# Kernel tuning notes

Hardware: AMD Instinct MI355X
Metric: run time of the kernel (lower is better)

## Reference

```python
import jax, jax.numpy as jnp
import numpy as np

B, N, C, K = 4, 4096, 64, 16
EPS = 1e-5


def _bn(x, g, b, m, v):
    # eval-mode BatchNorm2d on [B, C, N, K]
    scale = (g / jnp.sqrt(v + EPS))[None, :, None, None]
    return (x - m[None, :, None, None]) * scale + b[None, :, None, None]


def setup_inputs() -> dict:
    key = jax.random.key(0)
    ks = jax.random.split(key, 32)
    s = 0.05
    inp = {
        "p": jax.random.normal(ks[0], (B, N, 3), jnp.float32),
        "x": jax.random.normal(ks[1], (B, C, N), jnp.float32),
        "mask": jnp.ones((B, N), dtype=bool),
        # q/k/v 1x1 Conv1d weights [out, in] + bias
        "Wq": jax.random.normal(ks[2], (C, C)) * s, "bq": jax.random.normal(ks[3], (C,)) * s,
        "Wk": jax.random.normal(ks[4], (C, C)) * s, "bk": jax.random.normal(ks[5], (C,)) * s,
        "Wv": jax.random.normal(ks[6], (C, C)) * s, "bv": jax.random.normal(ks[7], (C,)) * s,
        # pos-enc: Conv2d(3->C, no bias), BN, ReLU, Conv2d(C->C)
        "pe_w1": jax.random.normal(ks[8], (C, 3)) * s,
        "pe_bn_g": jax.random.normal(ks[9], (C,)) * s + 1.0,
        "pe_bn_b": jax.random.normal(ks[10], (C,)) * s,
        "pe_bn_m": jax.random.normal(ks[11], (C,)) * s,
        "pe_bn_v": jax.random.uniform(ks[12], (C,), minval=0.5, maxval=1.5),
        "pe_w2": jax.random.normal(ks[13], (C, C)) * s, "pe_b2": jax.random.normal(ks[14], (C,)) * s,
        # attn: BN, ReLU, Conv2d(C->C, no bias), BN, ReLU, Conv2d(C->C)
        "at_bn0_g": jax.random.normal(ks[15], (C,)) * s + 1.0,
        "at_bn0_b": jax.random.normal(ks[16], (C,)) * s,
        "at_bn0_m": jax.random.normal(ks[17], (C,)) * s,
        "at_bn0_v": jax.random.uniform(ks[18], (C,), minval=0.5, maxval=1.5),
        "at_w1": jax.random.normal(ks[19], (C, C)) * s,
        "at_bn1_g": jax.random.normal(ks[20], (C,)) * s + 1.0,
        "at_bn1_b": jax.random.normal(ks[21], (C,)) * s,
        "at_bn1_m": jax.random.normal(ks[22], (C,)) * s,
        "at_bn1_v": jax.random.uniform(ks[23], (C,), minval=0.5, maxval=1.5),
        "at_w2": jax.random.normal(ks[24], (C, C)) * s, "at_b2": jax.random.normal(ks[25], (C,)) * s,
    }
    return inp


def reference(p, x, mask, Wq, bq, Wk, bk, Wv, bv,
              pe_w1, pe_bn_g, pe_bn_b, pe_bn_m, pe_bn_v, pe_w2, pe_b2,
              at_bn0_g, at_bn0_b, at_bn0_m, at_bn0_v, at_w1,
              at_bn1_g, at_bn1_b, at_bn1_m, at_bn1_v, at_w2, at_b2):
    # q, k, v: 1x1 Conv1d -> [B, C, N]
    q = jnp.einsum('oc,bcn->bon', Wq, x) + bq[None, :, None]
    k = jnp.einsum('oc,bcn->bon', Wk, x) + bk[None, :, None]
    v = jnp.einsum('oc,bcn->bon', Wv, x) + bv[None, :, None]

    # ---- knn_point(K, p, p): Euclidean cdist, zero-point masking, topk smallest
    sq = jnp.sum(p * p, axis=-1)                                   # [B, N]
    d2 = sq[:, :, None] + sq[:, None, :] - 2.0 * jnp.einsum('bnc,bmc->bnm', p, p)
    dist = jnp.sqrt(jnp.maximum(d2, 0.0))                          # [B, N, N]
    valid = ~jnp.all(p == 0, axis=-1)                              # [B, N]
    dist = jnp.where(valid[:, None, :], dist, jnp.inf)
    _, idx = jax.lax.top_k(-dist, K)                               # [B, N, K]

    gather = jax.vmap(lambda a, i: a[i])                           # ([N,C],[N,K]) -> [N,K,C]
    n_k = gather(jnp.transpose(k, (0, 2, 1)), idx)                 # [B, N, K, C]
    n_v = gather(jnp.transpose(v, (0, 2, 1)), idx)                 # [B, N, K, C]
    n_p = gather(p, idx)                                           # [B, N, K, 3]

    rel = p[:, :, None, :] - n_p                                   # [B, N, K, 3]
    rel = jnp.transpose(rel, (0, 3, 1, 2))                         # [B, 3, N, K]

    # position encoding MLP
    h = jnp.einsum('oc,bcnk->bonk', pe_w1, rel)
    h = jax.nn.relu(_bn(h, pe_bn_g, pe_bn_b, pe_bn_m, pe_bn_v))
    n_r = jnp.einsum('oc,bcnk->bonk', pe_w2, h) + pe_b2[None, :, None, None]  # [B,C,N,K]

    # attention MLP on (q - n_k + n_r)
    a = q[:, :, :, None] - jnp.transpose(n_k, (0, 3, 1, 2)) + n_r
    a = jax.nn.relu(_bn(a, at_bn0_g, at_bn0_b, at_bn0_m, at_bn0_v))
    a = jnp.einsum('oc,bcnk->bonk', at_w1, a)
    a = jax.nn.relu(_bn(a, at_bn1_g, at_bn1_b, at_bn1_m, at_bn1_v))
    a = jnp.einsum('oc,bcnk->bonk', at_w2, a) + at_b2[None, :, None, None]

    # mask [B,N] broadcast to [B,C,N,K] (masks query rows, as in original)
    a = jnp.where(mask[:, None, :, None], a, -1e10)
    a = jax.nn.softmax(a, axis=-1)
    a = jnp.where(jnp.isnan(a), 0.0, a)

    y = jnp.sum(a * (jnp.transpose(n_v, (0, 3, 1, 2)) + n_r), axis=-1)  # [B, C, N]
    return (p, y)
```

## Files before the change

kernel.cpp:

```cpp
#include <hip/hip_runtime.h>
#include <stdint.h>

#define NB 4
#define NP 4096
#define NC 64
#define NK 16
#define BN_EPS 1e-5f

typedef __attribute__((ext_vector_type(8))) short short8;
typedef __attribute__((ext_vector_type(4))) float f32x4;
typedef unsigned long long u64;

__device__ __forceinline__ short f2bf(float f) {
    unsigned u = __float_as_uint(f);
    unsigned r = (u + 0x7FFFu + ((u >> 16) & 1u)) >> 16;
    return (short)(unsigned short)r;
}

__global__ __launch_bounds__(256) void px_kernel(const float* __restrict__ p,
                                                 float4* __restrict__ px,
                                                 float* __restrict__ pcopy) {
    int gid = blockIdx.x * 256 + threadIdx.x;
    float x = p[gid * 3 + 0], y = p[gid * 3 + 1], z = p[gid * 3 + 2];
    pcopy[gid * 3 + 0] = x; pcopy[gid * 3 + 1] = y; pcopy[gid * 3 + 2] = z;
    float sq = fmaf(z, z, fmaf(y, y, x * x));
    bool inv = (x == 0.0f) && (y == 0.0f) && (z == 0.0f);
    px[gid] = make_float4(x, y, z, inv ? __builtin_inff() : sq);
}

__global__ __launch_bounds__(256) void qkv_kernel(
        const float* __restrict__ x,
        const float* __restrict__ Wq, const float* __restrict__ bq,
        const float* __restrict__ Wk, const float* __restrict__ bk,
        const float* __restrict__ Wv, const float* __restrict__ bv,
        float* __restrict__ outbase) {
    __shared__ float wt[NC * NC];
    __shared__ float bsh[NC];
    const int which = blockIdx.y;
    const float* W    = which == 0 ? Wq : which == 1 ? Wk : Wv;
    const float* bias = which == 0 ? bq : which == 1 ? bk : bv;
    float* out = outbase + (size_t)which * NB * NP * NC;

    for (int e = threadIdx.x; e < NC * NC; e += 256)
        wt[(e & 63) * NC + (e >> 6)] = W[e];
    if (threadIdx.x < NC) bsh[threadIdx.x] = bias[threadIdx.x];
    __syncthreads();

    const int gid   = blockIdx.x * 256 + threadIdx.x;
    const int token = gid & (NB * NP - 1);
    const int qtr   = gid >> 14;
    const int b = token >> 12, n = token & (NP - 1);

    float acc[16];
#pragma unroll
    for (int o = 0; o < 16; ++o) acc[o] = bsh[qtr * 16 + o];

    const float* xp = x + (size_t)b * NC * NP + n;
#pragma unroll 4
    for (int c = 0; c < NC; ++c) {
        float xc = xp[(size_t)c * NP];
        const float4* wr = (const float4*)&wt[c * NC + qtr * 16];
#pragma unroll
        for (int o4 = 0; o4 < 4; ++o4) {
            float4 w4 = wr[o4];
            acc[o4 * 4 + 0] = fmaf(w4.x, xc, acc[o4 * 4 + 0]);
            acc[o4 * 4 + 1] = fmaf(w4.y, xc, acc[o4 * 4 + 1]);
            acc[o4 * 4 + 2] = fmaf(w4.z, xc, acc[o4 * 4 + 2]);
            acc[o4 * 4 + 3] = fmaf(w4.w, xc, acc[o4 * 4 + 3]);
        }
    }
    float4* op = (float4*)(out + (size_t)token * NC + qtr * 16);
#pragma unroll
    for (int o4 = 0; o4 < 4; ++o4)
        op[o4] = make_float4(acc[o4 * 4 + 0], acc[o4 * 4 + 1],
                             acc[o4 * 4 + 2], acc[o4 * 4 + 3]);
}

#define KQW 4
#define KCAP 64

__global__ __launch_bounds__(256) void knn_kernel(const float4* __restrict__ px,
                                                  int* __restrict__ idxout) {
    __shared__ float tb[4][KQW * 64];
    __shared__ u64 sbuf[16][KCAP];
    __shared__ int scnt[16];
    const int l = threadIdx.x & 63;
    const int w = threadIdx.x >> 6;
    const int gw = blockIdx.x * 4 + w;
    const int q0 = gw * KQW;
    const int b  = q0 >> 12;
    const float4* pb = px + (size_t)b * NP;

    float4 pn[KQW];
#pragma unroll
    for (int j = 0; j < KQW; ++j) pn[j] = px[q0 + j];
    if (l < KQW) scnt[w * KQW + l] = 0;
    __builtin_amdgcn_wave_barrier();

    float k1[KQW];
#pragma unroll
    for (int j = 0; j < KQW; ++j) k1[j] = __builtin_inff();
#pragma unroll 4
    for (int i = 0; i < NP / 64; ++i) {
        float4 pm = pb[i * 64 + l];
#pragma unroll
        for (int j = 0; j < KQW; ++j) {
            float dot = fmaf(pm.z, pn[j].z, fmaf(pm.y, pn[j].y, pm.x * pn[j].x));
            float d2 = fmaxf((pn[j].w + pm.w) - 2.0f * dot, 0.0f);
            k1[j] = fminf(k1[j], d2);
        }
    }
#pragma unroll
    for (int j = 0; j < KQW; ++j) tb[w][j * 64 + l] = k1[j];
    __builtin_amdgcn_wave_barrier();

    float T[KQW];
#pragma unroll
    for (int j = 0; j < KQW; ++j) {
        const float* tj = &tb[w][j * 64];
        int rank = 0;
#pragma unroll 4
        for (int t = 0; t < 64; t += 4) {
            f32x4 v = *(const f32x4*)&tj[t];
            rank += (v[0] < k1[j]) + (v[1] < k1[j]) + (v[2] < k1[j]) + (v[3] < k1[j]);
        }
        float cand = (rank <= 15) ? k1[j] : -__builtin_inff();
#pragma unroll
        for (int off = 32; off; off >>= 1)
            cand = fmaxf(cand, __shfl_xor(cand, off));
        T[j] = cand;
    }

#pragma unroll 2
    for (int i = 0; i < NP / 64; ++i) {
        int m = i * 64 + l;
        float4 pm = pb[m];
#pragma unroll
        for (int j = 0; j < KQW; ++j) {
            float dot = fmaf(pm.z, pn[j].z, fmaf(pm.y, pn[j].y, pm.x * pn[j].x));
            float d2 = fmaxf((pn[j].w + pm.w) - 2.0f * dot, 0.0f);
            if (d2 <= T[j]) {
                int pos = atomicAdd(&scnt[w * KQW + j], 1);
                if (pos < KCAP)
                    sbuf[w * KQW + j][pos] =
                        ((u64)__float_as_uint(d2) << 32) | (unsigned int)m;
            }
        }
    }
    __builtin_amdgcn_wave_barrier();

#pragma unroll 1
    for (int j = 0; j < KQW; ++j) {
        int cnt = scnt[w * KQW + j];
        if (cnt > KCAP) cnt = KCAP;
        if (l < cnt) {
            const u64* sb = sbuf[w * KQW + j];
            u64 kj = sb[l];
            int rank = 0;
            for (int t = 0; t < cnt; ++t) rank += (sb[t] < kj);
            if (rank < NK)
                idxout[(size_t)(q0 + j) * NK + rank] = (int)(kj & 0xffffffffu);
        }
    }
}

#define QPW 4
#define HBSTR 72
#define DBSTR 20

__device__ __forceinline__ short8 pack8(float4 a, float4 b) {
    short8 r;
    r[0] = f2bf(a.x); r[1] = f2bf(a.y); r[2] = f2bf(a.z); r[3] = f2bf(a.w);
    r[4] = f2bf(b.x); r[5] = f2bf(b.y); r[6] = f2bf(b.z); r[7] = f2bf(b.w);
    return r;
}

__device__ __forceinline__ void gemm_stage(const short8* wf ,
                                           const unsigned short* HBw,
                                           float* DBw, int tok, int quad) {
    short8 b0 = *(const short8*)((const char*)HBw + tok * (HBSTR * 2) + quad * 16);
    short8 b1 = *(const short8*)((const char*)HBw + tok * (HBSTR * 2) + 64 + quad * 16);
#pragma unroll
    for (int ob = 0; ob < 4; ++ob) {
        f32x4 acc = {0.0f, 0.0f, 0.0f, 0.0f};
        acc = __builtin_amdgcn_mfma_f32_16x16x32_bf16(wf[ob * 2 + 0], b0, acc, 0, 0, 0);
        acc = __builtin_amdgcn_mfma_f32_16x16x32_bf16(wf[ob * 2 + 1], b1, acc, 0, 0, 0);
#pragma unroll
        for (int r = 0; r < 4; ++r)
            DBw[(ob * 16 + quad * 4 + r) * DBSTR + tok] = acc[r];
    }
}

__global__ __launch_bounds__(64, 2) void fused_mfma_kernel(
        const float4* __restrict__ px, const int* __restrict__ idx,
        const float* __restrict__ qT, const float* __restrict__ kT,
        const float* __restrict__ vT,
        const float* __restrict__ pe_w1,
        const float* __restrict__ pe_g, const float* __restrict__ pe_b,
        const float* __restrict__ pe_m, const float* __restrict__ pe_v,
        const float* __restrict__ pe_w2, const float* __restrict__ pe_b2,
        const float* __restrict__ b0g, const float* __restrict__ b0b,
        const float* __restrict__ b0m, const float* __restrict__ b0v,
        const float* __restrict__ at_w1,
        const float* __restrict__ b1g, const float* __restrict__ b1b,
        const float* __restrict__ b1m, const float* __restrict__ b1v,
        const float* __restrict__ at_w2, const float* __restrict__ at_b2,
        float* __restrict__ yout) {
    __shared__ __align__(16) unsigned short HBw[16 * HBSTR];
    __shared__ __align__(16) float DBw[64 * DBSTR];

    const int l    = threadIdx.x;
    const int c    = l;
    const int tok  = l & 15;
    const int quad = l >> 4;

    short8 wf[3][8];
    {
        const float* Ws[3] = {pe_w2, at_w1, at_w2};
#pragma unroll
        for (int mat = 0; mat < 3; ++mat)
#pragma unroll
            for (int ob = 0; ob < 4; ++ob)
#pragma unroll
                for (int ch = 0; ch < 2; ++ch) {
                    const float* src = Ws[mat] + (ob * 16 + tok) * NC + ch * 32 + quad * 8;
                    float4 a = *(const float4*)src;
                    float4 bq4 = *(const float4*)(src + 4);
                    wf[mat][ob * 2 + ch] = pack8(a, bq4);
                }
    }

    const float pw0 = pe_w1[c * 3 + 0], pw1 = pe_w1[c * 3 + 1], pw2v = pe_w1[c * 3 + 2];
    const float pes = pe_g[c] / sqrtf(pe_v[c] + BN_EPS);
    const float peb = fmaf(-pe_m[c], pes, pe_b[c]);
    const float s0  = b0g[c] / sqrtf(b0v[c] + BN_EPS);
    const float bb0 = fmaf(-b0m[c], s0, b0b[c]);
    const float s1  = b1g[c] / sqrtf(b1v[c] + BN_EPS);
    const float bb1 = fmaf(-b1m[c], s1, b1b[c]);
    const float peb2 = pe_b2[c];
    const float ab2  = at_b2[c];

    const int gw = blockIdx.x;

    for (int jq = 0; jq < QPW; ++jq) {
        const int qi = gw * QPW + jq;
        const int b = qi >> 12, n = qi & (NP - 1);
        const float4 pn = px[qi];
        const float qv = qT[(size_t)qi * NC + c];

        const int4* ip = (const int4*)(idx + (size_t)qi * NK);
        int4 nid0 = ip[0], nid1 = ip[1], nid2 = ip[2], nid3 = ip[3];
        int mreg[NK] = {nid0.x, nid0.y, nid0.z, nid0.w,
                        nid1.x, nid1.y, nid1.z, nid1.w,
                        nid2.x, nid2.y, nid2.z, nid2.w,
                        nid3.x, nid3.y, nid3.z, nid3.w};

        float4 pmr[NK];
#pragma unroll
        for (int k = 0; k < NK; ++k) pmr[k] = px[b * NP + mreg[k]];

#pragma unroll
        for (int k = 0; k < NK; ++k) {
            float r0 = pn.x - pmr[k].x, r1 = pn.y - pmr[k].y, r2 = pn.z - pmr[k].z;
            float h = fmaf(pw2v, r2, fmaf(pw1, r1, pw0 * r0));
            h = fmaxf(fmaf(h, pes, peb), 0.0f);
            HBw[k * HBSTR + c] = (unsigned short)f2bf(h);
        }
        __builtin_amdgcn_wave_barrier();

        float kreg[NK];
#pragma unroll
        for (int k = 0; k < NK; ++k)
            kreg[k] = kT[((size_t)(b * NP + mreg[k])) * NC + c];

        gemm_stage(wf[0], HBw, DBw, tok, quad);
        __builtin_amdgcn_wave_barrier();

        float nr[NK];
#pragma unroll
        for (int j = 0; j < 4; ++j) {
            f32x4 v4 = *(const f32x4*)(DBw + c * DBSTR + j * 4);
            nr[j * 4 + 0] = v4[0] + peb2;
            nr[j * 4 + 1] = v4[1] + peb2;
            nr[j * 4 + 2] = v4[2] + peb2;
            nr[j * 4 + 3] = v4[3] + peb2;
        }
        __builtin_amdgcn_wave_barrier();

#pragma unroll
        for (int k = 0; k < NK; ++k) {
            float a0 = qv - kreg[k] + nr[k];
            a0 = fmaxf(fmaf(a0, s0, bb0), 0.0f);
            HBw[k * HBSTR + c] = (unsigned short)f2bf(a0);
        }
        __builtin_amdgcn_wave_barrier();

        float vreg[NK];
#pragma unroll
        for (int k = 0; k < NK; ++k)
            vreg[k] = vT[((size_t)(b * NP + mreg[k])) * NC + c];

        gemm_stage(wf[1], HBw, DBw, tok, quad);
        __builtin_amdgcn_wave_barrier();

#pragma unroll
        for (int j = 0; j < 4; ++j) {
            f32x4 v4 = *(const f32x4*)(DBw + c * DBSTR + j * 4);
#pragma unroll
            for (int r = 0; r < 4; ++r) {
                float a2 = fmaxf(fmaf(v4[r], s1, bb1), 0.0f);
                HBw[(j * 4 + r) * HBSTR + c] = (unsigned short)f2bf(a2);
            }
        }
        __builtin_amdgcn_wave_barrier();

        gemm_stage(wf[2], HBw, DBw, tok, quad);
        __builtin_amdgcn_wave_barrier();

        float a3[NK];
#pragma unroll
        for (int j = 0; j < 4; ++j) {
            f32x4 v4 = *(const f32x4*)(DBw + c * DBSTR + j * 4);
            a3[j * 4 + 0] = v4[0] + ab2;
            a3[j * 4 + 1] = v4[1] + ab2;
            a3[j * 4 + 2] = v4[2] + ab2;
            a3[j * 4 + 3] = v4[3] + ab2;
        }
        __builtin_amdgcn_wave_barrier();

        float mx = a3[0];
#pragma unroll
        for (int k = 1; k < NK; ++k) mx = fmaxf(mx, a3[k]);
        float ssum = 0.0f, yacc = 0.0f;
#pragma unroll
        for (int k = 0; k < NK; ++k) {
            float e = __expf(a3[k] - mx);
            ssum += e;
            yacc = fmaf(e, vreg[k] + nr[k], yacc);
        }
        yout[((size_t)(b * NC + c)) * NP + n] = yacc / ssum;
        __builtin_amdgcn_wave_barrier();
    }
}

extern "C" void kernel_launch(void* const* d_in, const int* in_sizes, int n_in,
                              void* d_out, int out_size, void* d_ws, size_t ws_size,
                              hipStream_t stream) {
    const float* p    = (const float*)d_in[0];
    const float* x    = (const float*)d_in[1];
    const float* Wq = (const float*)d_in[3];  const float* bq = (const float*)d_in[4];
    const float* Wk = (const float*)d_in[5];  const float* bk = (const float*)d_in[6];
    const float* Wv = (const float*)d_in[7];  const float* bv = (const float*)d_in[8];
    const float* pe_w1 = (const float*)d_in[9];
    const float* pe_g  = (const float*)d_in[10]; const float* pe_b = (const float*)d_in[11];
    const float* pe_m  = (const float*)d_in[12]; const float* pe_v = (const float*)d_in[13];
    const float* pe_w2 = (const float*)d_in[14]; const float* pe_b2 = (const float*)d_in[15];
    const float* b0g = (const float*)d_in[16]; const float* b0b = (const float*)d_in[17];
    const float* b0m = (const float*)d_in[18]; const float* b0v = (const float*)d_in[19];
    const float* at_w1 = (const float*)d_in[20];
    const float* b1g = (const float*)d_in[21]; const float* b1b = (const float*)d_in[22];
    const float* b1m = (const float*)d_in[23]; const float* b1v = (const float*)d_in[24];
    const float* at_w2 = (const float*)d_in[25]; const float* at_b2 = (const float*)d_in[26];

    const size_t BNC = (size_t)NB * NP * NC;
    float* ws  = (float*)d_ws;
    float* qT  = ws;
    float* kT  = qT + BNC;
    float* vT  = kT + BNC;
    float4* px = (float4*)(vT + BNC);
    int* idx   = (int*)(px + (size_t)NB * NP);

    float* outp = (float*)d_out;
    float* y = outp + (size_t)NB * NP * 3;

    px_kernel<<<dim3(64), dim3(256), 0, stream>>>(p, px, outp);
    qkv_kernel<<<dim3(256, 3), dim3(256), 0, stream>>>(x, Wq, bq, Wk, bk, Wv, bv, qT);
    knn_kernel<<<dim3(1024), dim3(256), 0, stream>>>(px, idx);
    fused_mfma_kernel<<<dim3(4096), dim3(64), 0, stream>>>(
        px, idx, qT, kT, vT, pe_w1, pe_g, pe_b, pe_m, pe_v, pe_w2, pe_b2,
        b0g, b0b, b0m, b0v, at_w1, b1g, b1b, b1m, b1v, at_w2, at_b2, y);
}
```

Baseline: 225.8 us.

## Share bf16 weight fragments in LDS across four waves per block

The fused kernel now runs 256-thread blocks of four waves. Three of the waves cooperatively pack the three 64x64 weight matrices into bf16 MFMA fragments in LDS, and every wave reads its A operands from there instead of holding 24 short8 fragments in registers. This frees registers to raise occupancy and amortises the weight loads across four waves. Smaller changes split the neighbour-point gather into two halves, recompute the final logits from LDS instead of keeping a 16-float array, and remap queries so a block covers a single batch. In exchange it adds LDS reads for the weights on every MFMA and a block-wide barrier after setup.

```diff
diff --git a/kernel.cpp b/kernel.cpp
--- a/kernel.cpp
+++ b/kernel.cpp
@@ -175,23 +175,26 @@
     return r;
 }
 
-__device__ __forceinline__ void gemm_stage(const short8* wf ,
-                                           const unsigned short* HBw,
-                                           float* DBw, int tok, int quad) {
+__device__ __forceinline__ void gemm_stage_lds(const short8 (*__restrict__ WFm)[64],
+                                               int l,
+                                               const unsigned short* HBw,
+                                               float* DBw, int tok, int quad) {
     short8 b0 = *(const short8*)((const char*)HBw + tok * (HBSTR * 2) + quad * 16);
     short8 b1 = *(const short8*)((const char*)HBw + tok * (HBSTR * 2) + 64 + quad * 16);
 #pragma unroll
     for (int ob = 0; ob < 4; ++ob) {
         f32x4 acc = {0.0f, 0.0f, 0.0f, 0.0f};
-        acc = __builtin_amdgcn_mfma_f32_16x16x32_bf16(wf[ob * 2 + 0], b0, acc, 0, 0, 0);
-        acc = __builtin_amdgcn_mfma_f32_16x16x32_bf16(wf[ob * 2 + 1], b1, acc, 0, 0, 0);
+        short8 a0 = WFm[ob * 2 + 0][l];
+        short8 a1 = WFm[ob * 2 + 1][l];
+        acc = __builtin_amdgcn_mfma_f32_16x16x32_bf16(a0, b0, acc, 0, 0, 0);
+        acc = __builtin_amdgcn_mfma_f32_16x16x32_bf16(a1, b1, acc, 0, 0, 0);
 #pragma unroll
         for (int r = 0; r < 4; ++r)
             DBw[(ob * 16 + quad * 4 + r) * DBSTR + tok] = acc[r];
     }
 }
 
-__global__ __launch_bounds__(64, 2) void fused_mfma_kernel(
+__global__ __launch_bounds__(256, 3) void fused_mfma_kernel(
         const float4* __restrict__ px, const int* __restrict__ idx,
         const float* __restrict__ qT, const float* __restrict__ kT,
         const float* __restrict__ vT,
@@ -206,28 +209,26 @@
         const float* __restrict__ b1m, const float* __restrict__ b1v,
         const float* __restrict__ at_w2, const float* __restrict__ at_b2,
         float* __restrict__ yout) {
-    __shared__ __align__(16) unsigned short HBw[16 * HBSTR];
-    __shared__ __align__(16) float DBw[64 * DBSTR];
-
-    const int l    = threadIdx.x;
+    __shared__ __align__(16) short8 WFl[3][8][64];
+    __shared__ __align__(16) char UB[4][64 * DBSTR * 4];
+
+    const int l    = threadIdx.x & 63;
+    const int w    = threadIdx.x >> 6;
     const int c    = l;
     const int tok  = l & 15;
     const int quad = l >> 4;
 
-    short8 wf[3][8];
-    {
-        const float* Ws[3] = {pe_w2, at_w1, at_w2};
-#pragma unroll
-        for (int mat = 0; mat < 3; ++mat)
-#pragma unroll
-            for (int ob = 0; ob < 4; ++ob)
-#pragma unroll
-                for (int ch = 0; ch < 2; ++ch) {
-                    const float* src = Ws[mat] + (ob * 16 + tok) * NC + ch * 32 + quad * 8;
-                    float4 a = *(const float4*)src;
-                    float4 bq4 = *(const float4*)(src + 4);
-                    wf[mat][ob * 2 + ch] = pack8(a, bq4);
-                }
+    if (w < 3) {
+        const float* Wm = w == 0 ? pe_w2 : w == 1 ? at_w1 : at_w2;
+#pragma unroll
+        for (int ob = 0; ob < 4; ++ob)
+#pragma unroll
+            for (int ch = 0; ch < 2; ++ch) {
+                const float* src = Wm + (ob * 16 + tok) * NC + ch * 32 + quad * 8;
+                float4 a = *(const float4*)src;
+                float4 bq4 = *(const float4*)(src + 4);
+                WFl[w][ob * 2 + ch][l] = pack8(a, bq4);
+            }
     }
 
     const float pw0 = pe_w1[c * 3 + 0], pw1 = pe_w1[c * 3 + 1], pw2v = pe_w1[c * 3 + 2];
@@ -240,10 +241,17 @@
     const float peb2 = pe_b2[c];
     const float ab2  = at_b2[c];
 
-    const int gw = blockIdx.x;
+    __syncthreads();
+
+    unsigned short* HBw = (unsigned short*)UB[w];
+    float* DBw = (float*)UB[w];
+
+    const int batch = blockIdx.x & 3;
+    const int gwb   = (blockIdx.x >> 2) * 4 + w;
+    const int q0s   = batch * NP + gwb * QPW;
 
     for (int jq = 0; jq < QPW; ++jq) {
-        const int qi = gw * QPW + jq;
+        const int qi = q0s + jq;
         const int b = qi >> 12, n = qi & (NP - 1);
         const float4 pn = px[qi];
         const float qv = qT[(size_t)qi * NC + c];
@@ -255,16 +263,20 @@
                         nid2.x, nid2.y, nid2.z, nid2.w,
                         nid3.x, nid3.y, nid3.z, nid3.w};
 
-        float4 pmr[NK];
-#pragma unroll
-        for (int k = 0; k < NK; ++k) pmr[k] = px[b * NP + mreg[k]];
-
-#pragma unroll
-        for (int k = 0; k < NK; ++k) {
-            float r0 = pn.x - pmr[k].x, r1 = pn.y - pmr[k].y, r2 = pn.z - pmr[k].z;
-            float h = fmaf(pw2v, r2, fmaf(pw1, r1, pw0 * r0));
-            h = fmaxf(fmaf(h, pes, peb), 0.0f);
-            HBw[k * HBSTR + c] = (unsigned short)f2bf(h);
+        const float4* pxb = px + (size_t)b * NP;
+
+#pragma unroll
+        for (int h8 = 0; h8 < 2; ++h8) {
+            float4 pmr[8];
+#pragma unroll
+            for (int k = 0; k < 8; ++k) pmr[k] = pxb[mreg[h8 * 8 + k]];
+#pragma unroll
+            for (int k = 0; k < 8; ++k) {
+                float r0 = pn.x - pmr[k].x, r1 = pn.y - pmr[k].y, r2 = pn.z - pmr[k].z;
+                float h = fmaf(pw2v, r2, fmaf(pw1, r1, pw0 * r0));
+                h = fmaxf(fmaf(h, pes, peb), 0.0f);
+                HBw[(h8 * 8 + k) * HBSTR + c] = (unsigned short)f2bf(h);
+            }
         }
         __builtin_amdgcn_wave_barrier();
 
@@ -273,7 +285,7 @@
         for (int k = 0; k < NK; ++k)
             kreg[k] = kT[((size_t)(b * NP + mreg[k])) * NC + c];
 
-        gemm_stage(wf[0], HBw, DBw, tok, quad);
+        gemm_stage_lds(WFl[0], l, HBw, DBw, tok, quad);
         __builtin_amdgcn_wave_barrier();
 
         float nr[NK];
@@ -300,43 +312,45 @@
         for (int k = 0; k < NK; ++k)
             vreg[k] = vT[((size_t)(b * NP + mreg[k])) * NC + c];
 
-        gemm_stage(wf[1], HBw, DBw, tok, quad);
-        __builtin_amdgcn_wave_barrier();
-
+        gemm_stage_lds(WFl[1], l, HBw, DBw, tok, quad);
+        __builtin_amdgcn_wave_barrier();
+
+        float a1r[NK];
 #pragma unroll
         for (int j = 0; j < 4; ++j) {
             f32x4 v4 = *(const f32x4*)(DBw + c * DBSTR + j * 4);
-#pragma unroll
-            for (int r = 0; r < 4; ++r) {
-                float a2 = fmaxf(fmaf(v4[r], s1, bb1), 0.0f);
-                HBw[(j * 4 + r) * HBSTR + c] = (unsigned short)f2bf(a2);
-            }
-        }
-        __builtin_amdgcn_wave_barrier();
-
-        gemm_stage(wf[2], HBw, DBw, tok, quad);
-        __builtin_amdgcn_wave_barrier();
-
-        float a3[NK];
+            a1r[j * 4 + 0] = v4[0]; a1r[j * 4 + 1] = v4[1];
+            a1r[j * 4 + 2] = v4[2]; a1r[j * 4 + 3] = v4[3];
+        }
+        __builtin_amdgcn_wave_barrier();
+#pragma unroll
+        for (int k = 0; k < NK; ++k) {
+            float a2 = fmaxf(fmaf(a1r[k], s1, bb1), 0.0f);
+            HBw[k * HBSTR + c] = (unsigned short)f2bf(a2);
+        }
+        __builtin_amdgcn_wave_barrier();
+
+        gemm_stage_lds(WFl[2], l, HBw, DBw, tok, quad);
+        __builtin_amdgcn_wave_barrier();
+
+        float mxr = -__builtin_inff();
 #pragma unroll
         for (int j = 0; j < 4; ++j) {
             f32x4 v4 = *(const f32x4*)(DBw + c * DBSTR + j * 4);
-            a3[j * 4 + 0] = v4[0] + ab2;
-            a3[j * 4 + 1] = v4[1] + ab2;
-            a3[j * 4 + 2] = v4[2] + ab2;
-            a3[j * 4 + 3] = v4[3] + ab2;
-        }
-        __builtin_amdgcn_wave_barrier();
-
-        float mx = a3[0];
-#pragma unroll
-        for (int k = 1; k < NK; ++k) mx = fmaxf(mx, a3[k]);
+            mxr = fmaxf(mxr, fmaxf(fmaxf(v4[0], v4[1]), fmaxf(v4[2], v4[3])));
+        }
+        const float mx = mxr + ab2;
         float ssum = 0.0f, yacc = 0.0f;
 #pragma unroll
-        for (int k = 0; k < NK; ++k) {
-            float e = __expf(a3[k] - mx);
-            ssum += e;
-            yacc = fmaf(e, vreg[k] + nr[k], yacc);
+        for (int j = 0; j < 4; ++j) {
+            f32x4 v4 = *(const f32x4*)(DBw + c * DBSTR + j * 4);
+#pragma unroll
+            for (int r = 0; r < 4; ++r) {
+                const int k = j * 4 + r;
+                float e = __expf((v4[r] + ab2) - mx);
+                ssum += e;
+                yacc = fmaf(e, vreg[k] + nr[k], yacc);
+            }
         }
         yout[((size_t)(b * NC + c)) * NP + n] = yacc / ssum;
         __builtin_amdgcn_wave_barrier();
@@ -376,7 +390,7 @@
     px_kernel<<<dim3(64), dim3(256), 0, stream>>>(p, px, outp);
     qkv_kernel<<<dim3(256, 3), dim3(256), 0, stream>>>(x, Wq, bq, Wk, bk, Wv, bv, qT);
     knn_kernel<<<dim3(1024), dim3(256), 0, stream>>>(px, idx);
-    fused_mfma_kernel<<<dim3(4096), dim3(64), 0, stream>>>(
+    fused_mfma_kernel<<<dim3(1024), dim3(256), 0, stream>>>(
         px, idx, qT, kT, vT, pe_w1, pe_g, pe_b, pe_m, pe_v, pe_w2, pe_b2,
         b0g, b0b, b0m, b0v, at_w1, b1g, b1b, b1m, b1v, at_w2, at_b2, y);
 }
```

Result: faster. 205.6 us (-8.9%).
